# Optimization experiments

Measured on AMD Instinct MI355X. Metric: run time of the kernel, lower is better.

## Reference

```python
import jax, jax.numpy as jnp
import numpy as np

B, N = 16384, 1024


def _bit_reversal_indices(n):
    bits = int(np.log2(n))
    val = np.arange(n)
    src = np.zeros(n, dtype=np.int64)
    for _ in range(bits):
        src = (src << 1) | (val & 1)
        val = val >> 1
    return src  # src[k] = source pair for target pair k


def _inter_stage_indices(n, stage_idx):
    prev = 2 ** stage_idx
    kb = np.arange(n // 2)
    g = kb // prev
    kw = kb % prev
    half = (kw >= prev // 2).astype(np.int64)
    off = kw % (prev // 2)
    nb = prev // 2
    sE = (2 * g) * nb + off
    sO = (2 * g + 1) * nb + off
    perm = np.empty(n, dtype=np.int64)
    perm[2 * kb] = 2 * sE + half
    perm[2 * kb + 1] = 2 * sO + half
    return perm


def _final_unscramble_indices(n):
    k = np.arange(n // 2)
    perm = np.empty(n, dtype=np.int64)
    perm[k] = 2 * k
    perm[k + n // 2] = 2 * k + 1
    return perm


def _butterfly_weights(n, stage_idx):
    # grouped 1x1 conv weights -> (n//2, 4, 4): out = W[g] @ in per group
    Nb = 2 ** (stage_idx + 1)
    nub = Nb // 2
    reps = n // Nb
    k = np.arange(nub)
    rW = np.cos(2.0 * np.pi * k / Nb)      # Re(W_Nb^k)
    iW = -np.sin(2.0 * np.pi * k / Nb)     # Im(W_Nb^k) (forward DFT twiddle)
    W = np.zeros((nub, 4, 4), dtype=np.float32)
    W[:, 0, 0] = 1.0; W[:, 0, 2] = rW;  W[:, 0, 3] = -iW
    W[:, 1, 1] = 1.0; W[:, 1, 2] = iW;  W[:, 1, 3] = rW
    W[:, 2, 0] = 1.0; W[:, 2, 2] = -rW; W[:, 2, 3] = iW
    W[:, 3, 1] = 1.0; W[:, 3, 2] = -iW; W[:, 3, 3] = -rW
    return np.tile(W, (reps, 1, 1))  # (n//2, 4, 4)


def setup_inputs() -> dict:
    key = jax.random.key(0)
    x = jax.random.normal(key, (B, 2 * N, 1, 1), dtype=jnp.float32)
    return {"x": x}


def reference(x) -> jnp.ndarray:
    b = x.shape[0]
    n = x.shape[1] // 2
    stages = int(np.log2(n))
    # pairs view: (B, N, 2) = interleaved [Re, Im]
    v = x.reshape(b, n, 2)
    v = v[:, jnp.asarray(_bit_reversal_indices(n)), :]
    for s in range(stages):
        if s > 0:
            v = v[:, jnp.asarray(_inter_stage_indices(n, s)), :]
        W = jnp.asarray(_butterfly_weights(n, s))       # (N/2, 4, 4)
        g = v.reshape(b, n // 2, 4)                     # 4 channels per group
        g = jnp.einsum('goi,bgi->bgo', W, g)            # grouped 1x1 conv
        v = g.reshape(b, n, 2)
    v = v[:, jnp.asarray(_final_unscramble_indices(n)), :]
    return v.reshape(b, 2 * n, 1, 1)
```

## Files before the change

kernel.cpp:

```cpp
#include <hip/hip_runtime.h>

#define NFFT 1024
#define TPB 256
#define ROWS 4

__device__ __forceinline__ float2 cmul(float2 a, float2 b) {
  return make_float2(fmaf(a.x, b.x, -a.y * b.y), fmaf(a.x, b.y, a.y * b.x));
}
__device__ __forceinline__ float2 cadd(float2 a, float2 b) { return make_float2(a.x + b.x, a.y + b.y); }
__device__ __forceinline__ float2 csub(float2 a, float2 b) { return make_float2(a.x - b.x, a.y - b.y); }

__device__ __forceinline__ void dft4(const float2 v[4], float2 y[4]) {
  float2 s02 = cadd(v[0], v[2]), d02 = csub(v[0], v[2]);
  float2 s13 = cadd(v[1], v[3]), d13 = csub(v[1], v[3]);
  y[0] = cadd(s02, s13);
  y[2] = csub(s02, s13);
  y[1] = make_float2(d02.x + d13.y, d02.y - d13.x);
  y[3] = make_float2(d02.x - d13.y, d02.y + d13.x);
}

__device__ __forceinline__ float dpp_xor2(float x) {
  return __int_as_float(__builtin_amdgcn_update_dpp(0, __float_as_int(x), 0x4E, 0xF, 0xF, true));
}
__device__ __forceinline__ float dpp_xor1(float x) {
  return __int_as_float(__builtin_amdgcn_update_dpp(0, __float_as_int(x), 0xB1, 0xF, 0xF, true));
}

__device__ __forceinline__ void fft16(float2 z[16]) {
  float2 g[16];
  #pragma unroll
  for (int c0 = 0; c0 < 4; ++c0) {
    float2 v[4] = {z[c0], z[c0 + 4], z[c0 + 8], z[c0 + 12]};
    float2 y[4];
    dft4(v, y);
    g[4 * c0 + 0] = y[0]; g[4 * c0 + 1] = y[1]; g[4 * c0 + 2] = y[2]; g[4 * c0 + 3] = y[3];
  }
  const float C1 = 0.92387953251128674f, S1 = 0.38268343236508978f, R = 0.70710678118654752f;
  g[5]  = cmul(g[5],  make_float2( C1, -S1));
  g[6]  = cmul(g[6],  make_float2(  R,  -R));
  g[7]  = cmul(g[7],  make_float2( S1, -C1));
  g[9]  = cmul(g[9],  make_float2(  R,  -R));
  g[10] = make_float2(g[10].y, -g[10].x);
  g[11] = cmul(g[11], make_float2( -R,  -R));
  g[13] = cmul(g[13], make_float2( S1, -C1));
  g[14] = cmul(g[14], make_float2( -R,  -R));
  g[15] = cmul(g[15], make_float2(-C1,  S1));
  #pragma unroll
  for (int k0 = 0; k0 < 4; ++k0) {
    float2 v[4] = {g[k0], g[4 + k0], g[8 + k0], g[12 + k0]};
    float2 y[4];
    dft4(v, y);
    z[4 * k0 + 0] = y[0]; z[4 * k0 + 1] = y[1]; z[4 * k0 + 2] = y[2]; z[4 * k0 + 3] = y[3];
  }
}

__device__ __forceinline__ void twiddle_apply(float2 z[16], float2 u) {
  float2 w = u;
  #pragma unroll
  for (int k = 1; k < 16; ++k) {
    const int s = ((k & 3) << 2) | (k >> 2);
    z[s] = cmul(z[s], w);
    w = cmul(w, u);
  }
}

__device__ __forceinline__ void loadrow(float2 z[16], const float2* __restrict__ src, int lane) {
  #pragma unroll
  for (int c = 0; c < 16; ++c) z[c] = src[lane + 64 * c];
}

__device__ __forceinline__ void procrow(float2 z[16], float2* __restrict__ buf,
                                        float2 u1, float2 u2, int lane,
                                        float2* __restrict__ dst) {
  fft16(z);
  twiddle_apply(z, u1);

  const int m = lane >> 2, p = lane & 3;
  #pragma unroll
  for (int s = 0; s < 16; ++s) {
    const int kap = (s >> 2) | ((s & 3) << 2);
    buf[m * 64 + ((p + 4 * kap) ^ ((m & 3) << 2))] = z[s];
  }
  asm volatile("s_waitcnt lgkmcnt(0)" ::: "memory");
  __builtin_amdgcn_sched_barrier(0);
  #pragma unroll
  for (int mm = 0; mm < 16; ++mm) z[mm] = buf[mm * 64 + (lane ^ ((mm & 3) << 2))];

  fft16(z);
  twiddle_apply(z, u2);

  const float sgn1 = (lane & 2) ? -1.0f : 1.0f;
  const float sgn2 = (lane & 1) ? -1.0f : 1.0f;
  const bool tw3 = ((lane & 3) == 3);
  #pragma unroll
  for (int s = 0; s < 16; ++s) {
    float px = dpp_xor2(z[s].x), py = dpp_xor2(z[s].y);
    float ax = fmaf(sgn1, z[s].x, px), ay = fmaf(sgn1, z[s].y, py);
    float bx = tw3 ? ay : ax;
    float by = tw3 ? -ax : ay;
    float qx = dpp_xor1(bx), qy = dpp_xor1(by);
    z[s].x = fmaf(sgn2, bx, qx);
    z[s].y = fmaf(sgn2, by, qy);
  }

  const int kap = lane >> 2;
  const int ur = ((p & 1) << 1) | (p >> 1);
  float2* __restrict__ orow = dst + kap + 256 * ur;
  #pragma unroll
  for (int s = 0; s < 16; ++s) {
    const int t = (s >> 2) | ((s & 3) << 2);
    __builtin_nontemporal_store(*reinterpret_cast<const double*>(&z[s]),
                                reinterpret_cast<double*>(orow + 16 * t));
  }
}

__global__ __launch_bounds__(TPB, 4) void fft1024_kernel(const float* __restrict__ in,
                                                         float* __restrict__ out,
                                                         int nrows) {
  __shared__ float2 lds[TPB / 64][NFFT];
  const int wv = threadIdx.x >> 6;
  const int lane = threadIdx.x & 63;
  const int r0 = (blockIdx.x * (TPB / 64) + wv) * ROWS;
  if (r0 >= nrows) return;

  const float2* __restrict__ xin = reinterpret_cast<const float2*>(in) + (size_t)r0 * NFFT;
  float2* __restrict__ xout = reinterpret_cast<float2*>(out) + (size_t)r0 * NFFT;
  float2* buf = lds[wv];

  float sn, cs;
  __sincosf((float)lane * (-6.2831853071795864769f / 1024.0f), &sn, &cs);
  const float2 u1 = make_float2(cs, sn);
  __sincosf((float)(lane & 3) * (-6.2831853071795864769f / 64.0f), &sn, &cs);
  const float2 u2 = make_float2(cs, sn);

  float2 A[16], B[16];
  loadrow(A, xin, lane);
  loadrow(B, xin + NFFT, lane);
  procrow(A, buf, u1, u2, lane, xout);
  loadrow(A, xin + 2 * NFFT, lane);
  procrow(B, buf, u1, u2, lane, xout + NFFT);
  loadrow(B, xin + 3 * NFFT, lane);
  procrow(A, buf, u1, u2, lane, xout + 2 * NFFT);
  procrow(B, buf, u1, u2, lane, xout + 3 * NFFT);
}

extern "C" void kernel_launch(void* const* d_in, const int* in_sizes, int n_in,
                              void* d_out, int out_size, void* d_ws, size_t ws_size,
                              hipStream_t stream) {
  const float* x = (const float*)d_in[0];
  float* out = (float*)d_out;
  const int rows = in_sizes[0] / (2 * NFFT);
  const int rpb = (TPB / 64) * ROWS;
  const int blocks = (rows + rpb - 1) / rpb;
  fft1024_kernel<<<blocks, TPB, 0, stream>>>(x, out, rows);
}
```

Before: 271.8 us.

## Halve rows per wave, shorten twiddle chain, and use plain stores

Each wave now processes two FFT rows instead of four, which doubles the grid and drops the software-pipelined load of the next row during compute. The twiddle multiply switches from one serial power chain to four interleaved chains stepped by u^4, giving shorter dependency chains at a small cost in accuracy. Output stores become ordinary stores instead of nontemporal ones, and a wait is added after the LDS reads. These are several independent tweaks at once: lower per-wave latency hiding traded for more waves, plus changes to cache behaviour on the write path.

```diff
diff --git a/kernel.cpp b/kernel.cpp
--- a/kernel.cpp
+++ b/kernel.cpp
@@ -2,7 +2,7 @@
 
 #define NFFT 1024
 #define TPB 256
-#define ROWS 4
+#define RPW 2
 
 __device__ __forceinline__ float2 cmul(float2 a, float2 b) {
   return make_float2(fmaf(a.x, b.x, -a.y * b.y), fmaf(a.x, b.y, a.y * b.x));
@@ -55,18 +55,19 @@
 }
 
 __device__ __forceinline__ void twiddle_apply(float2 z[16], float2 u) {
-  float2 w = u;
-  #pragma unroll
-  for (int k = 1; k < 16; ++k) {
-    const int s = ((k & 3) << 2) | (k >> 2);
-    z[s] = cmul(z[s], w);
-    w = cmul(w, u);
-  }
-}
-
-__device__ __forceinline__ void loadrow(float2 z[16], const float2* __restrict__ src, int lane) {
-  #pragma unroll
-  for (int c = 0; c < 16; ++c) z[c] = src[lane + 64 * c];
+  const float2 u2 = cmul(u, u);
+  const float2 u4 = cmul(u2, u2);
+  float2 c1 = u, c2 = u2, c3 = cmul(u2, u), c4 = u4;
+  z[4]  = cmul(z[4],  c1); z[8]  = cmul(z[8],  c2);
+  z[12] = cmul(z[12], c3); z[1]  = cmul(z[1],  c4);
+  c1 = cmul(c1, u4); c2 = cmul(c2, u4); c3 = cmul(c3, u4); c4 = cmul(c4, u4);
+  z[5]  = cmul(z[5],  c1); z[9]  = cmul(z[9],  c2);
+  z[13] = cmul(z[13], c3); z[2]  = cmul(z[2],  c4);
+  c1 = cmul(c1, u4); c2 = cmul(c2, u4); c3 = cmul(c3, u4); c4 = cmul(c4, u4);
+  z[6]  = cmul(z[6],  c1); z[10] = cmul(z[10], c2);
+  z[14] = cmul(z[14], c3); z[3]  = cmul(z[3],  c4);
+  c1 = cmul(c1, u4); c2 = cmul(c2, u4); c3 = cmul(c3, u4);
+  z[7]  = cmul(z[7],  c1); z[11] = cmul(z[11], c2); z[15] = cmul(z[15], c3);
 }
 
 __device__ __forceinline__ void procrow(float2 z[16], float2* __restrict__ buf,
@@ -85,6 +86,8 @@
   __builtin_amdgcn_sched_barrier(0);
   #pragma unroll
   for (int mm = 0; mm < 16; ++mm) z[mm] = buf[mm * 64 + (lane ^ ((mm & 3) << 2))];
+  asm volatile("s_waitcnt lgkmcnt(0)" ::: "memory");
+  __builtin_amdgcn_sched_barrier(0);
 
   fft16(z);
   twiddle_apply(z, u2);
@@ -109,18 +112,17 @@
   #pragma unroll
   for (int s = 0; s < 16; ++s) {
     const int t = (s >> 2) | ((s & 3) << 2);
-    __builtin_nontemporal_store(*reinterpret_cast<const double*>(&z[s]),
-                                reinterpret_cast<double*>(orow + 16 * t));
+    orow[16 * t] = z[s];
   }
 }
 
 __global__ __launch_bounds__(TPB, 4) void fft1024_kernel(const float* __restrict__ in,
                                                          float* __restrict__ out,
                                                          int nrows) {
-  __shared__ float2 lds[TPB / 64][NFFT];
+  __shared__ __align__(16) float2 lds[TPB / 64][NFFT];
   const int wv = threadIdx.x >> 6;
   const int lane = threadIdx.x & 63;
-  const int r0 = (blockIdx.x * (TPB / 64) + wv) * ROWS;
+  const int r0 = (blockIdx.x * (TPB / 64) + wv) * RPW;
   if (r0 >= nrows) return;
 
   const float2* __restrict__ xin = reinterpret_cast<const float2*>(in) + (size_t)r0 * NFFT;
@@ -134,14 +136,12 @@
   const float2 u2 = make_float2(cs, sn);
 
   float2 A[16], B[16];
-  loadrow(A, xin, lane);
-  loadrow(B, xin + NFFT, lane);
+  #pragma unroll
+  for (int c = 0; c < 16; ++c) A[c] = xin[lane + 64 * c];
+  #pragma unroll
+  for (int c = 0; c < 16; ++c) B[c] = xin[NFFT + lane + 64 * c];
   procrow(A, buf, u1, u2, lane, xout);
-  loadrow(A, xin + 2 * NFFT, lane);
   procrow(B, buf, u1, u2, lane, xout + NFFT);
-  loadrow(B, xin + 3 * NFFT, lane);
-  procrow(A, buf, u1, u2, lane, xout + 2 * NFFT);
-  procrow(B, buf, u1, u2, lane, xout + 3 * NFFT);
 }
 
 extern "C" void kernel_launch(void* const* d_in, const int* in_sizes, int n_in,
@@ -150,7 +150,7 @@
   const float* x = (const float*)d_in[0];
   float* out = (float*)d_out;
   const int rows = in_sizes[0] / (2 * NFFT);
-  const int rpb = (TPB / 64) * ROWS;
+  const int rpb = (TPB / 64) * RPW;
   const int blocks = (rows + rpb - 1) / rpb;
   fft1024_kernel<<<blocks, TPB, 0, stream>>>(x, out, rows);
 }
```

Result: faster. 241.1 us (-11.3%).
